# Kernel optimization log

Measured on AMD Instinct MI355X. Metric: run time of the kernel, lower is better.

## Reference

```python
import jax, jax.numpy as jnp
import numpy as np

STRIDE = 16
A = 9
PRE_NMS_TOP_N = 6000
POST_NMS_TOP_N = 300
NMS_THRESH = 0.7
MIN_SIZE = 16
H, W = 128, 192


def _generate_anchors(base_size=16, ratios=(0.5, 1.0, 2.0), scales=(8, 16, 32)):
    base = np.array([0, 0, base_size - 1, base_size - 1], dtype=np.float64)
    w = base[2] - base[0] + 1
    h = base[3] - base[1] + 1
    x_ctr = base[0] + 0.5 * (w - 1)
    y_ctr = base[1] + 0.5 * (h - 1)
    size = w * h
    ratios = np.array(ratios)
    ws = np.round(np.sqrt(size / ratios))
    hs = np.round(ws * ratios)
    ratio_anchors = np.stack([x_ctr - 0.5 * (ws - 1), y_ctr - 0.5 * (hs - 1),
                              x_ctr + 0.5 * (ws - 1), y_ctr + 0.5 * (hs - 1)], axis=1)
    out = []
    scales = np.array(scales)
    for a in ratio_anchors:
        aw = a[2] - a[0] + 1
        ah = a[3] - a[1] + 1
        xc = a[0] + 0.5 * (aw - 1)
        yc = a[1] + 0.5 * (ah - 1)
        ws2 = aw * scales
        hs2 = ah * scales
        out.append(np.stack([xc - 0.5 * (ws2 - 1), yc - 0.5 * (hs2 - 1),
                             xc + 0.5 * (ws2 - 1), yc + 0.5 * (hs2 - 1)], axis=1))
    return np.concatenate(out, axis=0).astype(np.float32)  # [9,4]


def setup_inputs() -> dict:
    key = jax.random.key(0)
    k1, k2 = jax.random.split(key)
    scores = jax.random.uniform(k1, (1, 2 * A, H, W), dtype=jnp.float32)
    bbox_deltas = 0.1 * jax.random.normal(k2, (1, 4 * A, H, W), dtype=jnp.float32)
    im_info = jnp.array([[H * STRIDE, W * STRIDE, 1.0]], dtype=jnp.float32)
    return {"scores": scores, "bbox_deltas": bbox_deltas, "im_info": im_info}


def _proposal_forward(scores, bbox_deltas, im_info):
    anchors_base = jnp.asarray(_generate_anchors())  # [A,4]
    sc = scores[:, A:, :, :]                          # fg scores [1,A,H,W]
    h, w = sc.shape[-2], sc.shape[-1]
    shift_x = (jnp.arange(w) * STRIDE).astype(sc.dtype)
    shift_y = (jnp.arange(h) * STRIDE).astype(sc.dtype)
    sy, sx = jnp.meshgrid(shift_y, shift_x, indexing='ij')
    shifts = jnp.stack([sx.ravel(), sy.ravel(), sx.ravel(), sy.ravel()], axis=1)  # [K,4]
    anchors = (anchors_base[None, :, :] + shifts[:, None, :]).reshape(-1, 4)      # [K*A,4]

    deltas = bbox_deltas.transpose(0, 2, 3, 1).reshape(-1, 4)
    deltas = jnp.concatenate([deltas[:, :2], jnp.clip(deltas[:, 2:], -10.0, 10.0)], axis=1)
    sc = sc.transpose(0, 2, 3, 1).reshape(-1)  # [K*A]

    widths = anchors[:, 2] - anchors[:, 0] + 1.0
    heights = anchors[:, 3] - anchors[:, 1] + 1.0
    ctr_x = anchors[:, 0] + 0.5 * widths
    ctr_y = anchors[:, 1] + 0.5 * heights
    dx, dy, dw, dh = deltas[:, 0], deltas[:, 1], deltas[:, 2], deltas[:, 3]
    pcx = dx * widths + ctr_x
    pcy = dy * heights + ctr_y
    pw = jnp.exp(dw) * widths
    ph = jnp.exp(dh) * heights
    x1 = pcx - 0.5 * pw
    y1 = pcy - 0.5 * ph
    x2 = pcx + 0.5 * pw
    y2 = pcy + 0.5 * ph

    info = im_info[0]
    x1 = jnp.clip(x1, 0.0, info[1] - 1.0)
    x2 = jnp.clip(x2, 0.0, info[1] - 1.0)
    y1 = jnp.clip(y1, 0.0, info[0] - 1.0)
    y2 = jnp.clip(y2, 0.0, info[0] - 1.0)
    proposals = jnp.stack([x1, y1, x2, y2], axis=1)

    # filter_boxes: mask (instead of dropping) boxes smaller than min_size*scale
    min_sz = MIN_SIZE * info[2]
    valid = ((x2 - x1 + 1.0) >= min_sz) & ((y2 - y1 + 1.0) >= min_sz)
    masked = jnp.where(valid, sc, -jnp.inf)

    # sort desc + pre_nms_topN
    top_scores, top_idx = jax.lax.top_k(masked, PRE_NMS_TOP_N)
    boxes = proposals[top_idx]               # [PRE,4], score-descending
    tvalid = top_scores > -jnp.inf

    # pairwise IoU (torchvision convention)
    area = (boxes[:, 2] - boxes[:, 0]) * (boxes[:, 3] - boxes[:, 1])
    lt = jnp.maximum(boxes[:, None, :2], boxes[None, :, :2])
    rb = jnp.minimum(boxes[:, None, 2:], boxes[None, :, 2:])
    wh = jnp.clip(rb - lt, 0.0)
    inter = wh[..., 0] * wh[..., 1]
    iou = inter / (area[:, None] + area[None, :] - inter)  # [PRE,PRE]

    # greedy NMS over score-sorted boxes
    n = PRE_NMS_TOP_N
    def step(keep, x):
        iou_col, v, i = x
        suppressed = jnp.any(keep & (iou_col > NMS_THRESH))
        k = v & jnp.logical_not(suppressed)
        keep = keep.at[i].set(k)
        return keep, k
    keep, _ = jax.lax.scan(step, jnp.zeros((n,), dtype=bool),
                           (iou.T, tvalid, jnp.arange(n)))

    # kept boxes first (stable => score order preserved), take post_nms_topN
    order = jnp.argsort(jnp.logical_not(keep).astype(jnp.int32), stable=True)[:POST_NMS_TOP_N]
    kept = keep[order]
    out_boxes = jnp.where(kept[:, None], boxes[order], 0.0)
    output = jnp.concatenate(
        [jnp.zeros((POST_NMS_TOP_N, 1), out_boxes.dtype), out_boxes], axis=1)
    return output  # [POST,5]: (batch_idx=0, x1,y1,x2,y2); rows beyond kept count are zero


def reference(scores, bbox_deltas, im_info):
    return _proposal_forward(scores, bbox_deltas, im_info)
```

## Files before the change

kernel.cpp:

```cpp
#include <hip/hip_runtime.h>

#define N_ANCH 221184
#define HW     24576
#define Wd     192
#define AA     9
#define TOPN   6000
#define POSTN  300
#define CAND_CAP 8192
#define RJ     2048
#define NWORDS 94

typedef unsigned long long u64;

__device__ const float c_aw[9] = {184.f,368.f,736.f,128.f,256.f,512.f, 88.f,176.f,352.f};
__device__ const float c_ah[9] = { 96.f,192.f,384.f,128.f,256.f,512.f,176.f,352.f,704.f};

#define Z1_F4 10420
#define Z2_F4 2048
__global__ __launch_bounds__(256) void init_kernel(float4* z1, float4* z2) {
    int t = blockIdx.x * 256 + threadIdx.x;
    if (t < Z1_F4) {
        if (t == 256) ((int4*)z1)[t] = make_int4(0, TOPN, 0, 0);
        else z1[t] = make_float4(0.f, 0.f, 0.f, 0.f);
    } else if (t < Z1_F4 + Z2_F4) {
        z2[t - Z1_F4] = make_float4(0.f, 0.f, 0.f, 0.f);
    }
}

__global__ __launch_bounds__(256) void decode_kernel(const float* __restrict__ scores,
                                                     const float* __restrict__ deltas,
                                                     const float* __restrict__ iminfo,
                                                     float4* __restrict__ boxesj,
                                                     unsigned int* __restrict__ keys,
                                                     unsigned int* __restrict__ hist_r1) {
    __shared__ unsigned int lh[256];
    lh[threadIdx.x] = 0u;
    __syncthreads();

    int t = blockIdx.x * 256 + threadIdx.x;
    {
        int a = t / HW;
        int cell = t - a * HW;
        int h = cell / Wd;
        int w = cell - h * Wd;

        float score = scores[(AA + a) * HW + cell];
        const float* db = deltas + (size_t)(4 * a) * HW + cell;
        float dx = db[0];
        float dy = db[HW];
        float dw = db[2 * HW];
        float dh = db[3 * HW];
        dw = fminf(fmaxf(dw, -10.f), 10.f);
        dh = fminf(fmaxf(dh, -10.f), 10.f);

        float ww = c_aw[a], hh = c_ah[a];
        float cx = 16.f * (float)w + 8.f;
        float cy = 16.f * (float)h + 8.f;

        float pcx = __fadd_rn(__fmul_rn(dx, ww), cx);
        float pcy = __fadd_rn(__fmul_rn(dy, hh), cy);
        float pw  = __fmul_rn(expf(dw), ww);
        float ph  = __fmul_rn(expf(dh), hh);
        float hpw = __fmul_rn(0.5f, pw);
        float hph = __fmul_rn(0.5f, ph);
        float x1 = __fsub_rn(pcx, hpw);
        float x2 = __fadd_rn(pcx, hpw);
        float y1 = __fsub_rn(pcy, hph);
        float y2 = __fadd_rn(pcy, hph);

        float info0 = iminfo[0], info1 = iminfo[1], info2 = iminfo[2];
        float xmax = __fsub_rn(info1, 1.f);
        float ymax = __fsub_rn(info0, 1.f);
        x1 = fminf(fmaxf(x1, 0.f), xmax);
        x2 = fminf(fmaxf(x2, 0.f), xmax);
        y1 = fminf(fmaxf(y1, 0.f), ymax);
        y2 = fminf(fmaxf(y2, 0.f), ymax);

        float msz = __fmul_rn(16.f, info2);
        bool valid = (__fadd_rn(__fsub_rn(x2, x1), 1.f) >= msz) &&
                     (__fadd_rn(__fsub_rn(y2, y1), 1.f) >= msz);

        unsigned int sb = __float_as_uint(score);
        unsigned int key = valid ? ((sb & 0x80000000u) ? ~sb : (sb | 0x80000000u))
                                 : 0x007FFFFFu;
        boxesj[t] = make_float4(x1, y1, x2, y2);
        keys[t] = key;
        atomicAdd(&lh[key >> 24], 1u);
    }
    __syncthreads();
    atomicAdd(&hist_r1[threadIdx.x], lh[threadIdx.x]);
}

__global__ __launch_bounds__(256) void hist_kernel(const unsigned int* __restrict__ keys,
                                                   const unsigned int* __restrict__ state,
                                                   unsigned int* __restrict__ hist,
                                                   int shift, unsigned int himask) {
    __shared__ unsigned int lh[256];
    lh[threadIdx.x] = 0u;
    __syncthreads();
    unsigned int pref = state[0];
    int t = blockIdx.x * 256 + threadIdx.x;
    {
        unsigned int k = keys[t];
        if ((k & himask) == (pref & himask))
            atomicAdd(&lh[(k >> shift) & 0xFFu], 1u);
    }
    __syncthreads();
    atomicAdd(&hist[threadIdx.x], lh[threadIdx.x]);
}

__global__ __launch_bounds__(256) void select_kernel(const unsigned int* __restrict__ hist,
                                                     unsigned int* __restrict__ state,
                                                     int shift) {
    __shared__ unsigned int s[256];
    int t = threadIdx.x;
    s[t] = hist[t];
    unsigned int rank = state[1];
    __syncthreads();
    for (int d = 1; d < 256; d <<= 1) {
        unsigned int v = (t + d < 256) ? s[t + d] : 0u;
        __syncthreads();
        s[t] += v;
        __syncthreads();
    }
    unsigned int ge = s[t];
    unsigned int gt = (t < 255) ? s[t + 1] : 0u;
    if (ge >= rank && gt < rank) {
        state[0] |= ((unsigned int)t) << shift;
        state[1] = rank - gt;
    }
}

__global__ __launch_bounds__(256) void compact_kernel(const unsigned int* __restrict__ keys,
                                                      unsigned int* __restrict__ state,
                                                      u64* __restrict__ cand) {
    int t = blockIdx.x * 256 + threadIdx.x;
    unsigned int k = keys[t];
    unsigned int T = state[0];
    if (k >= T) {
        unsigned int pos = atomicAdd(&state[2], 1u);
        if (pos < CAND_CAP) {
            int a = t / HW;
            int cell = t - a * HW;
            unsigned int aidx = (unsigned int)(cell * 9 + a);
            cand[pos] = ((u64)k << 32) | (u64)(~aidx);
        }
    }
}

__global__ __launch_bounds__(256) void rank_kernel(const u64* __restrict__ cand,
                                                   unsigned int* __restrict__ rank) {
    __shared__ u64 s[RJ];
    const u64* src = cand + (size_t)blockIdx.y * RJ;
    for (int j = threadIdx.x; j < RJ; j += 256) s[j] = src[j];
    int i = blockIdx.x * 256 + threadIdx.x;
    u64 k = cand[i];
    __syncthreads();
    unsigned int cnt = 0;
    #pragma unroll 16
    for (int j = 0; j < RJ; ++j) cnt += (s[j] > k) ? 1u : 0u;
    if (k != 0ull && cnt != 0u) atomicAdd(&rank[i], cnt);
}

__global__ __launch_bounds__(256) void scatter_kernel(const u64* __restrict__ cand,
                                                      const unsigned int* __restrict__ rank,
                                                      const float4* __restrict__ boxesj,
                                                      float4* __restrict__ tb,
                                                      u64* __restrict__ vmask) {
    int i = blockIdx.x * 256 + threadIdx.x;
    u64 k = cand[i];
    if (k == 0ull) return;
    unsigned int r = rank[i];
    if (r >= TOPN) return;
    unsigned int hi = (unsigned int)(k >> 32);
    unsigned int aidx = ~((unsigned int)k);
    int a = (int)(aidx % 9u);
    int cell = (int)(aidx / 9u);
    tb[r] = boxesj[(size_t)a * HW + cell];
    if (hi != 0x007FFFFFu) atomicOr(&vmask[r >> 6], 1ull << (r & 63));
}

__global__ __launch_bounds__(64) void nms_matrix_kernel(const float4* __restrict__ tb,
                                                        u64* __restrict__ mat) {
    if (blockIdx.x < blockIdx.y) return;
    __shared__ float4 cb[64];
    int t = threadIdx.x;
    int c0 = blockIdx.x * 64;
    int col = c0 + t;
    cb[t] = (col < TOPN) ? tb[col] : make_float4(0.f, 0.f, 0.f, 0.f);
    __syncthreads();
    int row = blockIdx.y * 64 + t;
    if (row >= TOPN) return;
    float4 rb = tb[row];
    float rA = (rb.z - rb.x) * (rb.w - rb.y);
    u64 mask = 0ull;
    for (int c = 0; c < 64; ++c) {
        if (c0 + c >= TOPN) break;
        float4 b = cb[c];
        float lx = fmaxf(rb.x, b.x), ly = fmaxf(rb.y, b.y);
        float rx = fminf(rb.z, b.z), ry = fminf(rb.w, b.w);
        float iw = fmaxf(rx - lx, 0.f), ih = fmaxf(ry - ly, 0.f);
        float inter = iw * ih;
        float bA = (b.z - b.x) * (b.w - b.y);
        float iou = inter / ((rA + bA) - inter);
        if (iou > 0.7f) mask |= (1ull << c);
    }
    mat[(size_t)row * NWORDS + blockIdx.x] = mask;
}

__global__ __launch_bounds__(64) void nms_scan_kernel(const u64* __restrict__ mat,
                                                      const u64* __restrict__ vmask,
                                                      const float4* __restrict__ tb,
                                                      float* __restrict__ out) {
    int lane = threadIdx.x;
    u64 r0 = ~vmask[lane];
    u64 r1 = (lane < NWORDS - 64) ? ~vmask[64 + lane] : ~0ull;
    __shared__ int kept[POSTN];
    int cnt = 0;

    for (int c = 0; c < NWORDS && cnt < POSTN; ++c) {
        int i0 = c * 64 + lane;
        u64 intra = 0ull;
        if (i0 < TOPN) intra = mat[(size_t)i0 * NWORDS + c];

        u64 stat = (c < 64) ? __shfl(r0, c) : __shfl(r1, c - 64);
        if (stat == ~0ull) continue;

        u64 removed = stat;
        u64 keptmask = 0ull;
        while (removed != ~0ull && cnt < POSTN) {
            int b = __ffsll((u64)~removed) - 1;
            keptmask |= (1ull << b);
            if (lane == 0) kept[cnt] = c * 64 + b;
            ++cnt;
            removed |= __shfl(intra, b) | (1ull << b);
        }
        if (cnt >= POSTN) break;

        u64 f0 = 0ull, f1 = 0ull;
        u64 km = keptmask;
        while (km) {
            int bs[8];
            #pragma unroll
            for (int j = 0; j < 8; ++j) {
                bs[j] = km ? (__ffsll(km) - 1) : -1;
                if (km) km &= km - 1;
            }
            u64 v0[8], v1[8];
            #pragma unroll
            for (int j = 0; j < 8; ++j) {
                v0[j] = 0ull; v1[j] = 0ull;
                if (bs[j] >= 0) {
                    const u64* row = mat + (size_t)(c * 64 + bs[j]) * NWORDS;
                    if (lane > c) v0[j] = row[lane];
                    if (lane + 64 < NWORDS && lane + 64 > c) v1[j] = row[lane + 64];
                }
            }
            #pragma unroll
            for (int j = 0; j < 8; ++j) { f0 |= v0[j]; f1 |= v1[j]; }
        }
        r0 |= f0; r1 |= f1;
    }

    __syncthreads();
    for (int r = lane; r < POSTN; r += 64) {
        float4 b = make_float4(0.f, 0.f, 0.f, 0.f);
        if (r < cnt) b = tb[kept[r]];
        float* o = out + r * 5;
        o[0] = 0.f; o[1] = b.x; o[2] = b.y; o[3] = b.z; o[4] = b.w;
    }
}

extern "C" void kernel_launch(void* const* d_in, const int* in_sizes, int n_in,
                              void* d_out, int out_size, void* d_ws, size_t ws_size,
                              hipStream_t stream) {
    const float* scores = (const float*)d_in[0];
    const float* deltas = (const float*)d_in[1];
    const float* iminfo = (const float*)d_in[2];
    float* out = (float*)d_out;

    char* ws = (char*)d_ws;
    float4*             boxesj = (float4*)(ws + 0);
    unsigned int*       keys   = (unsigned int*)(ws + 3538944);
    unsigned int*       hist   = (unsigned int*)(ws + 4423680);
    unsigned int*       state  = (unsigned int*)(ws + 4427776);
    u64*                cand   = (u64*)(ws + 4427840);
    float4*             tb     = (float4*)(ws + 4493376);
    u64*                vmask  = (u64*)(ws + 4589632);
    u64*                mat    = (u64*)(ws + 4590400);
    unsigned int*       rankp  = (unsigned int*)mat;

    const int NB = N_ANCH / 256;

    init_kernel<<<49, 256, 0, stream>>>((float4*)(ws + 4423680), (float4*)mat);
    decode_kernel<<<NB, 256, 0, stream>>>(scores, deltas, iminfo, boxesj, keys, hist + 256);
    select_kernel<<<1, 256, 0, stream>>>(hist + 256, state, 24);
    hist_kernel<<<NB, 256, 0, stream>>>(keys, state, hist, 16, 0xFF000000u);
    select_kernel<<<1, 256, 0, stream>>>(hist, state, 16);
    compact_kernel<<<NB, 256, 0, stream>>>(keys, state, cand);
    rank_kernel<<<dim3(CAND_CAP / 256, CAND_CAP / RJ), 256, 0, stream>>>(cand, rankp);
    scatter_kernel<<<CAND_CAP / 256, 256, 0, stream>>>(cand, rankp, boxesj, tb, vmask);
    nms_matrix_kernel<<<dim3(NWORDS, NWORDS), 64, 0, stream>>>(tb, mat);
    nms_scan_kernel<<<1, 64, 0, stream>>>(mat, vmask, tb, out);
}
```

Baseline: 256.5 us.

## Fuse top-k selection stages, redecode boxes lazily, and restructure NMS scan

The decode kernel no longer writes all decoded boxes; only the top candidates are re-decoded inside a fused rank+scatter kernel. The two-pass 8-bit radix select becomes one 16-bit global histogram with a single 1024-thread select kernel. Rank and scatter merge into one kernel that splits each candidate's comparisons across two threads. The NMS scan now handles 128-box chunks with prefetched intra-chunk masks and readlane broadcasts. This removes several launches and the 3.5 MB box buffer, but adds global atomic contention on the 65536-bin histogram and repeats decode work.

New measurement: 351.1 us. +36.9%, slower.

```diff
diff --git a/kernel.cpp b/kernel.cpp
--- a/kernel.cpp
+++ b/kernel.cpp
@@ -7,127 +7,105 @@
 #define TOPN   6000
 #define POSTN  300
 #define CAND_CAP 8192
-#define RJ     2048
 #define NWORDS 94
+#define NCHUNK 47
 
 typedef unsigned long long u64;
 
 __device__ const float c_aw[9] = {184.f,368.f,736.f,128.f,256.f,512.f, 88.f,176.f,352.f};
 __device__ const float c_ah[9] = { 96.f,192.f,384.f,128.f,256.f,512.f,176.f,352.f,704.f};
 
-#define Z1_F4 10420
-#define Z2_F4 2048
-__global__ __launch_bounds__(256) void init_kernel(float4* z1, float4* z2) {
+__device__ __forceinline__ float4 decode_box(int a, int cell,
+                                             const float* __restrict__ deltas,
+                                             float info0, float info1, float info2,
+                                             bool* valid) {
+    int h = cell / Wd;
+    int w = cell - h * Wd;
+    const float* db = deltas + (size_t)(4 * a) * HW + cell;
+    float dx = db[0];
+    float dy = db[HW];
+    float dw = db[2 * HW];
+    float dh = db[3 * HW];
+    dw = fminf(fmaxf(dw, -10.f), 10.f);
+    dh = fminf(fmaxf(dh, -10.f), 10.f);
+
+    float ww = c_aw[a], hh = c_ah[a];
+    float cx = 16.f * (float)w + 8.f;
+    float cy = 16.f * (float)h + 8.f;
+
+    float pcx = __fadd_rn(__fmul_rn(dx, ww), cx);
+    float pcy = __fadd_rn(__fmul_rn(dy, hh), cy);
+    float pw  = __fmul_rn(expf(dw), ww);
+    float ph  = __fmul_rn(expf(dh), hh);
+    float hpw = __fmul_rn(0.5f, pw);
+    float hph = __fmul_rn(0.5f, ph);
+    float x1 = __fsub_rn(pcx, hpw);
+    float x2 = __fadd_rn(pcx, hpw);
+    float y1 = __fsub_rn(pcy, hph);
+    float y2 = __fadd_rn(pcy, hph);
+
+    float xmax = __fsub_rn(info1, 1.f);
+    float ymax = __fsub_rn(info0, 1.f);
+    x1 = fminf(fmaxf(x1, 0.f), xmax);
+    x2 = fminf(fmaxf(x2, 0.f), xmax);
+    y1 = fminf(fmaxf(y1, 0.f), ymax);
+    y2 = fminf(fmaxf(y2, 0.f), ymax);
+
+    float msz = __fmul_rn(16.f, info2);
+    *valid = (__fadd_rn(__fsub_rn(x2, x1), 1.f) >= msz) &&
+             (__fadd_rn(__fsub_rn(y2, y1), 1.f) >= msz);
+    return make_float4(x1, y1, x2, y2);
+}
+
+#define ZA_F4 20484
+#define ZB_F4 48
+__global__ __launch_bounds__(256) void init_kernel(float4* zA, float4* zB) {
     int t = blockIdx.x * 256 + threadIdx.x;
-    if (t < Z1_F4) {
-        if (t == 256) ((int4*)z1)[t] = make_int4(0, TOPN, 0, 0);
-        else z1[t] = make_float4(0.f, 0.f, 0.f, 0.f);
-    } else if (t < Z1_F4 + Z2_F4) {
-        z2[t - Z1_F4] = make_float4(0.f, 0.f, 0.f, 0.f);
-    }
+    float4 z = make_float4(0.f, 0.f, 0.f, 0.f);
+    if (t < ZA_F4) zA[t] = z;
+    else if (t < ZA_F4 + ZB_F4) zB[t - ZA_F4] = z;
 }
 
 __global__ __launch_bounds__(256) void decode_kernel(const float* __restrict__ scores,
                                                      const float* __restrict__ deltas,
                                                      const float* __restrict__ iminfo,
-                                                     float4* __restrict__ boxesj,
                                                      unsigned int* __restrict__ keys,
-                                                     unsigned int* __restrict__ hist_r1) {
-    __shared__ unsigned int lh[256];
-    lh[threadIdx.x] = 0u;
+                                                     unsigned int* __restrict__ hist16) {
+    int t = blockIdx.x * 256 + threadIdx.x;
+    int a = t / HW;
+    int cell = t - a * HW;
+    float score = scores[(AA + a) * HW + cell];
+    bool valid;
+    (void)decode_box(a, cell, deltas, iminfo[0], iminfo[1], iminfo[2], &valid);
+    unsigned int sb = __float_as_uint(score);
+    unsigned int key = valid ? ((sb & 0x80000000u) ? ~sb : (sb | 0x80000000u))
+                             : 0x007FFFFFu;
+    keys[t] = key;
+    atomicAdd(&hist16[key >> 16], 1u);
+}
+
+__global__ __launch_bounds__(1024) void select16_kernel(const unsigned int* __restrict__ hist,
+                                                        unsigned int* __restrict__ state) {
+    __shared__ unsigned int ssum[1024];
+    int t = threadIdx.x;
+    unsigned int local = 0;
+    for (int i = 0; i < 64; ++i) local += hist[t * 64 + i];
+    ssum[t] = local;
     __syncthreads();
-
-    int t = blockIdx.x * 256 + threadIdx.x;
-    {
-        int a = t / HW;
-        int cell = t - a * HW;
-        int h = cell / Wd;
-        int w = cell - h * Wd;
-
-        float score = scores[(AA + a) * HW + cell];
-        const float* db = deltas + (size_t)(4 * a) * HW + cell;
-        float dx = db[0];
-        float dy = db[HW];
-        float dw = db[2 * HW];
-        float dh = db[3 * HW];
-        dw = fminf(fmaxf(dw, -10.f), 10.f);
-        dh = fminf(fmaxf(dh, -10.f), 10.f);
-
-        float ww = c_aw[a], hh = c_ah[a];
-        float cx = 16.f * (float)w + 8.f;
-        float cy = 16.f * (float)h + 8.f;
-
-        float pcx = __fadd_rn(__fmul_rn(dx, ww), cx);
-        float pcy = __fadd_rn(__fmul_rn(dy, hh), cy);
-        float pw  = __fmul_rn(expf(dw), ww);
-        float ph  = __fmul_rn(expf(dh), hh);
-        float hpw = __fmul_rn(0.5f, pw);
-        float hph = __fmul_rn(0.5f, ph);
-        float x1 = __fsub_rn(pcx, hpw);
-        float x2 = __fadd_rn(pcx, hpw);
-        float y1 = __fsub_rn(pcy, hph);
-        float y2 = __fadd_rn(pcy, hph);
-
-        float info0 = iminfo[0], info1 = iminfo[1], info2 = iminfo[2];
-        float xmax = __fsub_rn(info1, 1.f);
-        float ymax = __fsub_rn(info0, 1.f);
-        x1 = fminf(fmaxf(x1, 0.f), xmax);
-        x2 = fminf(fmaxf(x2, 0.f), xmax);
-        y1 = fminf(fmaxf(y1, 0.f), ymax);
-        y2 = fminf(fmaxf(y2, 0.f), ymax);
-
-        float msz = __fmul_rn(16.f, info2);
-        bool valid = (__fadd_rn(__fsub_rn(x2, x1), 1.f) >= msz) &&
-                     (__fadd_rn(__fsub_rn(y2, y1), 1.f) >= msz);
-
-        unsigned int sb = __float_as_uint(score);
-        unsigned int key = valid ? ((sb & 0x80000000u) ? ~sb : (sb | 0x80000000u))
-                                 : 0x007FFFFFu;
-        boxesj[t] = make_float4(x1, y1, x2, y2);
-        keys[t] = key;
-        atomicAdd(&lh[key >> 24], 1u);
-    }
-    __syncthreads();
-    atomicAdd(&hist_r1[threadIdx.x], lh[threadIdx.x]);
-}
-
-__global__ __launch_bounds__(256) void hist_kernel(const unsigned int* __restrict__ keys,
-                                                   const unsigned int* __restrict__ state,
-                                                   unsigned int* __restrict__ hist,
-                                                   int shift, unsigned int himask) {
-    __shared__ unsigned int lh[256];
-    lh[threadIdx.x] = 0u;
-    __syncthreads();
-    unsigned int pref = state[0];
-    int t = blockIdx.x * 256 + threadIdx.x;
-    {
-        unsigned int k = keys[t];
-        if ((k & himask) == (pref & himask))
-            atomicAdd(&lh[(k >> shift) & 0xFFu], 1u);
-    }
-    __syncthreads();
-    atomicAdd(&hist[threadIdx.x], lh[threadIdx.x]);
-}
-
-__global__ __launch_bounds__(256) void select_kernel(const unsigned int* __restrict__ hist,
-                                                     unsigned int* __restrict__ state,
-                                                     int shift) {
-    __shared__ unsigned int s[256];
-    int t = threadIdx.x;
-    s[t] = hist[t];
-    unsigned int rank = state[1];
-    __syncthreads();
-    for (int d = 1; d < 256; d <<= 1) {
-        unsigned int v = (t + d < 256) ? s[t + d] : 0u;
+    for (int d = 1; d < 1024; d <<= 1) {
+        unsigned int v = (t + d < 1024) ? ssum[t + d] : 0u;
         __syncthreads();
-        s[t] += v;
+        ssum[t] += v;
         __syncthreads();
     }
-    unsigned int ge = s[t];
-    unsigned int gt = (t < 255) ? s[t + 1] : 0u;
-    if (ge >= rank && gt < rank) {
-        state[0] |= ((unsigned int)t) << shift;
-        state[1] = rank - gt;
+    unsigned int ge = ssum[t];
+    unsigned int gt = (t < 1023) ? ssum[t + 1] : 0u;
+    if (ge >= TOPN && gt < TOPN) {
+        unsigned int running = gt;
+        for (int i = 63; i >= 0; --i) {
+            running += hist[t * 64 + i];
+            if (running >= TOPN) { state[0] = ((unsigned int)(t * 64 + i)) << 16; break; }
+        }
     }
 }
 
@@ -148,36 +126,36 @@
     }
 }
 
-__global__ __launch_bounds__(256) void rank_kernel(const u64* __restrict__ cand,
-                                                   unsigned int* __restrict__ rank) {
-    __shared__ u64 s[RJ];
-    const u64* src = cand + (size_t)blockIdx.y * RJ;
-    for (int j = threadIdx.x; j < RJ; j += 256) s[j] = src[j];
-    int i = blockIdx.x * 256 + threadIdx.x;
+__global__ __launch_bounds__(256) void rank_scatter_kernel(const u64* __restrict__ cand,
+                                                           const float* __restrict__ deltas,
+                                                           const float* __restrict__ iminfo,
+                                                           float4* __restrict__ tb,
+                                                           u64* __restrict__ vmask) {
+    __shared__ u64 s[CAND_CAP];
+    for (int j = threadIdx.x; j < CAND_CAP; j += 256) s[j] = cand[j];
+    int half = threadIdx.x & 1;
+    int i = blockIdx.x * 128 + (threadIdx.x >> 1);
     u64 k = cand[i];
     __syncthreads();
+    const ulonglong2* sv = (const ulonglong2*)(s + half * (CAND_CAP / 2));
     unsigned int cnt = 0;
-    #pragma unroll 16
-    for (int j = 0; j < RJ; ++j) cnt += (s[j] > k) ? 1u : 0u;
-    if (k != 0ull && cnt != 0u) atomicAdd(&rank[i], cnt);
-}
-
-__global__ __launch_bounds__(256) void scatter_kernel(const u64* __restrict__ cand,
-                                                      const unsigned int* __restrict__ rank,
-                                                      const float4* __restrict__ boxesj,
-                                                      float4* __restrict__ tb,
-                                                      u64* __restrict__ vmask) {
-    int i = blockIdx.x * 256 + threadIdx.x;
-    u64 k = cand[i];
-    if (k == 0ull) return;
-    unsigned int r = rank[i];
-    if (r >= TOPN) return;
-    unsigned int hi = (unsigned int)(k >> 32);
-    unsigned int aidx = ~((unsigned int)k);
-    int a = (int)(aidx % 9u);
-    int cell = (int)(aidx / 9u);
-    tb[r] = boxesj[(size_t)a * HW + cell];
-    if (hi != 0x007FFFFFu) atomicOr(&vmask[r >> 6], 1ull << (r & 63));
+    #pragma unroll 8
+    for (int j = 0; j < CAND_CAP / 4; ++j) {
+        ulonglong2 v = sv[j];
+        cnt += (v.x > k) ? 1u : 0u;
+        cnt += (v.y > k) ? 1u : 0u;
+    }
+    cnt += __shfl_xor(cnt, 1);
+    if (half == 0 && k != 0ull && cnt < TOPN) {
+        unsigned int aidx = ~((unsigned int)k);
+        int a = (int)(aidx % 9u);
+        int cell = (int)(aidx / 9u);
+        bool valid;
+        float4 box = decode_box(a, cell, deltas, iminfo[0], iminfo[1], iminfo[2], &valid);
+        tb[cnt] = box;
+        if ((unsigned int)(k >> 32) != 0x007FFFFFu)
+            atomicOr(&vmask[cnt >> 6], 1ull << (cnt & 63));
+    }
 }
 
 __global__ __launch_bounds__(64) void nms_matrix_kernel(const float4* __restrict__ tb,
@@ -208,6 +186,12 @@
     mat[(size_t)row * NWORDS + blockIdx.x] = mask;
 }
 
+__device__ __forceinline__ u64 rdl64(u64 v, int l) {
+    unsigned int lo = (unsigned int)__builtin_amdgcn_readlane((int)(unsigned int)v, l);
+    unsigned int hi = (unsigned int)__builtin_amdgcn_readlane((int)(unsigned int)(v >> 32), l);
+    return ((u64)hi << 32) | (u64)lo;
+}
+
 __global__ __launch_bounds__(64) void nms_scan_kernel(const u64* __restrict__ mat,
                                                       const u64* __restrict__ vmask,
                                                       const float4* __restrict__ tb,
@@ -218,51 +202,74 @@
     __shared__ int kept[POSTN];
     int cnt = 0;
 
-    for (int c = 0; c < NWORDS && cnt < POSTN; ++c) {
-        int i0 = c * 64 + lane;
-        u64 intra = 0ull;
-        if (i0 < TOPN) intra = mat[(size_t)i0 * NWORDS + c];
-
-        u64 stat = (c < 64) ? __shfl(r0, c) : __shfl(r1, c - 64);
-        if (stat == ~0ull) continue;
-
-        u64 removed = stat;
-        u64 keptmask = 0ull;
-        while (removed != ~0ull && cnt < POSTN) {
-            int b = __ffsll((u64)~removed) - 1;
-            keptmask |= (1ull << b);
-            if (lane == 0) kept[cnt] = c * 64 + b;
-            ++cnt;
-            removed |= __shfl(intra, b) | (1ull << b);
+    u64 a0, a1, b0, b1;
+    {
+        ulonglong2 vA = *(const ulonglong2*)(mat + (size_t)lane * NWORDS);
+        ulonglong2 vB = *(const ulonglong2*)(mat + (size_t)(64 + lane) * NWORDS);
+        a0 = vA.x; a1 = vA.y; b0 = vB.x; b1 = vB.y;
+    }
+    for (int c = 0; c < NCHUNK; ++c) {
+        u64 na0 = 0, na1 = 0, nb0 = 0, nb1 = 0;
+        if (c + 1 < NCHUNK) {
+            const u64* pA = mat + (size_t)((c + 1) * 128 + lane) * NWORDS + 2 * (c + 1);
+            const u64* pB = mat + (size_t)((c + 1) * 128 + 64 + lane) * NWORDS + 2 * (c + 1);
+            ulonglong2 vA = *(const ulonglong2*)pA;
+            ulonglong2 vB = *(const ulonglong2*)pB;
+            na0 = vA.x; na1 = vA.y; nb0 = vB.x; nb1 = vB.y;
         }
-        if (cnt >= POSTN) break;
-
-        u64 f0 = 0ull, f1 = 0ull;
-        u64 km = keptmask;
-        while (km) {
-            int bs[8];
-            #pragma unroll
-            for (int j = 0; j < 8; ++j) {
-                bs[j] = km ? (__ffsll(km) - 1) : -1;
-                if (km) km &= km - 1;
+        int w2 = 2 * c;
+        u64 s0 = (w2 < 64) ? rdl64(r0, w2) : rdl64(r1, w2 - 64);
+        u64 s1 = (w2 + 1 < 64) ? rdl64(r0, w2 + 1) : rdl64(r1, w2 + 1 - 64);
+        if ((s0 & s1) != ~0ull) {
+            int base = c * 128;
+            u64 rem0 = s0, rem1 = s1, k0 = 0ull, k1 = 0ull;
+            while (cnt < POSTN) {
+                int b;
+                if (~rem0) b = __ffsll((u64)~rem0) - 1;
+                else if (~rem1) b = 64 + __ffsll((u64)~rem1) - 1;
+                else break;
+                if (lane == 0) kept[cnt] = base + b;
+                ++cnt;
+                u64 w0, w1;
+                if (b < 64) {
+                    w0 = rdl64(a0, b); w1 = rdl64(a1, b);
+                    k0 |= 1ull << b; rem0 |= 1ull << b;
+                } else {
+                    int bb = b - 64;
+                    w0 = rdl64(b0, bb); w1 = rdl64(b1, bb);
+                    k1 |= 1ull << bb; rem1 |= 1ull << bb;
+                }
+                rem0 |= w0; rem1 |= w1;
             }
-            u64 v0[8], v1[8];
-            #pragma unroll
-            for (int j = 0; j < 8; ++j) {
-                v0[j] = 0ull; v1[j] = 0ull;
-                if (bs[j] >= 0) {
-                    const u64* row = mat + (size_t)(c * 64 + bs[j]) * NWORDS;
-                    if (lane > c) v0[j] = row[lane];
-                    if (lane + 64 < NWORDS && lane + 64 > c) v1[j] = row[lane + 64];
+            if (cnt >= POSTN) break;
+            u64 f0 = 0ull, f1 = 0ull, m0 = k0, m1 = k1;
+            while (m0 | m1) {
+                int idxs[8];
+                #pragma unroll
+                for (int j = 0; j < 8; ++j) {
+                    int b = -1;
+                    if (m0) { b = __ffsll(m0) - 1; m0 &= m0 - 1; }
+                    else if (m1) { b = 64 + __ffsll(m1) - 1; m1 &= m1 - 1; }
+                    idxs[j] = b;
                 }
+                u64 v0[8], v1[8];
+                #pragma unroll
+                for (int j = 0; j < 8; ++j) {
+                    v0[j] = 0ull; v1[j] = 0ull;
+                    if (idxs[j] >= 0) {
+                        const u64* row = mat + (size_t)(base + idxs[j]) * NWORDS;
+                        v0[j] = row[lane];
+                        if (lane < NWORDS - 64) v1[j] = row[64 + lane];
+                    }
+                }
+                #pragma unroll
+                for (int j = 0; j < 8; ++j) { f0 |= v0[j]; f1 |= v1[j]; }
             }
-            #pragma unroll
-            for (int j = 0; j < 8; ++j) { f0 |= v0[j]; f1 |= v1[j]; }
+            r0 |= f0; r1 |= f1;
         }
-        r0 |= f0; r1 |= f1;
-    }
-
-    __syncthreads();
+        a0 = na0; a1 = na1; b0 = nb0; b1 = nb1;
+    }
+
     for (int r = lane; r < POSTN; r += 64) {
         float4 b = make_float4(0.f, 0.f, 0.f, 0.f);
         if (r < cnt) b = tb[kept[r]];
@@ -280,26 +287,21 @@
     float* out = (float*)d_out;
 
     char* ws = (char*)d_ws;
-    float4*             boxesj = (float4*)(ws + 0);
-    unsigned int*       keys   = (unsigned int*)(ws + 3538944);
-    unsigned int*       hist   = (unsigned int*)(ws + 4423680);
-    unsigned int*       state  = (unsigned int*)(ws + 4427776);
-    u64*                cand   = (u64*)(ws + 4427840);
-    float4*             tb     = (float4*)(ws + 4493376);
-    u64*                vmask  = (u64*)(ws + 4589632);
-    u64*                mat    = (u64*)(ws + 4590400);
-    unsigned int*       rankp  = (unsigned int*)mat;
+    unsigned int* keys   = (unsigned int*)(ws + 0);
+    unsigned int* hist16 = (unsigned int*)(ws + 884736);
+    unsigned int* state  = (unsigned int*)(ws + 1146880);
+    u64*          cand   = (u64*)(ws + 1146944);
+    float4*       tb     = (float4*)(ws + 1212480);
+    u64*          vmask  = (u64*)(ws + 1308736);
+    u64*          mat    = (u64*)(ws + 1309504);
 
     const int NB = N_ANCH / 256;
 
-    init_kernel<<<49, 256, 0, stream>>>((float4*)(ws + 4423680), (float4*)mat);
-    decode_kernel<<<NB, 256, 0, stream>>>(scores, deltas, iminfo, boxesj, keys, hist + 256);
-    select_kernel<<<1, 256, 0, stream>>>(hist + 256, state, 24);
-    hist_kernel<<<NB, 256, 0, stream>>>(keys, state, hist, 16, 0xFF000000u);
-    select_kernel<<<1, 256, 0, stream>>>(hist, state, 16);
+    init_kernel<<<81, 256, 0, stream>>>((float4*)hist16, (float4*)vmask);
+    decode_kernel<<<NB, 256, 0, stream>>>(scores, deltas, iminfo, keys, hist16);
+    select16_kernel<<<1, 1024, 0, stream>>>(hist16, state);
     compact_kernel<<<NB, 256, 0, stream>>>(keys, state, cand);
-    rank_kernel<<<dim3(CAND_CAP / 256, CAND_CAP / RJ), 256, 0, stream>>>(cand, rankp);
-    scatter_kernel<<<CAND_CAP / 256, 256, 0, stream>>>(cand, rankp, boxesj, tb, vmask);
+    rank_scatter_kernel<<<CAND_CAP / 128, 256, 0, stream>>>(cand, deltas, iminfo, tb, vmask);
     nms_matrix_kernel<<<dim3(NWORDS, NWORDS), 64, 0, stream>>>(tb, mat);
     nms_scan_kernel<<<1, 64, 0, stream>>>(mat, vmask, tb, out);
 }
```
